# Kernel tuning notes

Measured on AMD Instinct MI355X. Metric: run time of the kernel, lower is better.

Reference implementation:

```python
import jax, jax.numpy as jnp
import numpy as np

MAX_DIST = 3          # census patch radius -> 7x7 neighborhood
PATCH = 2 * MAX_DIST + 1


def _warp(img, flow):
    """Bilinear warp (Resample2d): sample img at (x + u, y + v). Coords clamped to border."""
    B, C, H, W = img.shape
    gy, gx = jnp.meshgrid(jnp.arange(H, dtype=img.dtype), jnp.arange(W, dtype=img.dtype), indexing='ij')
    x = gx[None] + flow[:, 0]           # [B,H,W]
    y = gy[None] + flow[:, 1]
    x0 = jnp.floor(x); y0 = jnp.floor(y)
    wx = x - x0; wy = y - y0            # bilinear weights
    x0i = jnp.clip(x0, 0, W - 1).astype(jnp.int32)
    x1i = jnp.clip(x0 + 1.0, 0, W - 1).astype(jnp.int32)
    y0i = jnp.clip(y0, 0, H - 1).astype(jnp.int32)
    y1i = jnp.clip(y0 + 1.0, 0, H - 1).astype(jnp.int32)

    def gather(im_b, yi, xi):           # im_b [C,H,W], yi/xi [H,W] -> [C,H,W]
        return im_b[:, yi, xi]
    g = jax.vmap(gather)
    Ia = g(img, y0i, x0i); Ib = g(img, y0i, x1i)
    Ic = g(img, y1i, x0i); Id = g(img, y1i, x1i)
    wx = wx[:, None]; wy = wy[:, None]  # [B,1,H,W]
    return Ia * (1 - wx) * (1 - wy) + Ib * wx * (1 - wy) + Ic * (1 - wx) * wy + Id * wx * wy


def _census_transform(image):
    """Ternary census transform: grayscale, extract 7x7 patches, normalized center differences."""
    gray = (0.299 * image[:, 0:1] + 0.587 * image[:, 1:2] + 0.114 * image[:, 2:3]) * 255.0
    w = jnp.eye(PATCH * PATCH, dtype=image.dtype).reshape(PATCH * PATCH, 1, PATCH, PATCH)
    patches = jax.lax.conv_general_dilated(
        gray, w, window_strides=(1, 1), padding=[(MAX_DIST, MAX_DIST)] * 2,
        dimension_numbers=('NCHW', 'OIHW', 'NCHW'))   # [B,49,H,W]
    t = patches - gray
    return t / jnp.sqrt(0.81 + t * t)


def _border_mask(B, H, W, dtype):
    m = jnp.zeros((H, W), dtype).at[MAX_DIST:H - MAX_DIST, MAX_DIST:W - MAX_DIST].set(1.0)
    return jnp.broadcast_to(m[None, None], (B, 1, H, W))


def _charbonnier(x, mask, alpha=0.45, eps=0.001):
    err = (x * x + eps * eps) ** alpha * mask
    return jnp.sum(err) / x.size


def _census_loss(im1, im2_warped, mask):
    t1 = _census_transform(im1)
    t2 = _census_transform(im2_warped)
    d = (t1 - t2) ** 2
    dist = jnp.sum(d / (0.1 + d), axis=1, keepdims=True)   # soft Hamming distance [B,1,H,W]
    B, _, H, W = dist.shape
    return _charbonnier(dist, mask * _border_mask(B, H, W, dist.dtype))


def setup_inputs() -> dict:
    key = jax.random.key(0)
    ks = jax.random.split(key, 6)
    B, H, W = 4, 320, 768
    return {
        'former': jax.random.uniform(ks[0], (B, 3, H, W), jnp.float32),
        'latter': jax.random.uniform(ks[1], (B, 3, H, W), jnp.float32),
        'disp_est_scale': jax.random.normal(ks[2], (B, 2, H, W), jnp.float32) * 3.0,
        'disp_est_scale_2': jax.random.normal(ks[3], (B, 2, H, W), jnp.float32) * 3.0,
        'fw_mask': jax.random.uniform(ks[4], (B, 1, H, W), jnp.float32),
        'bw_mask': jax.random.uniform(ks[5], (B, 1, H, W), jnp.float32),
    }


def reference(former, latter, disp_est_scale, disp_est_scale_2, fw_mask, bw_mask):
    left_est = _warp(latter, disp_est_scale)
    image_loss = _census_loss(former, left_est, fw_mask)
    right_est = _warp(former, disp_est_scale_2)
    image_loss_2 = _census_loss(latter, right_est, bw_mask)
    return (image_loss, image_loss_2)
```

## Files before the change

### kernel.cpp

```cpp
#include <hip/hip_runtime.h>

#define BB 4
#define H 320
#define W 768
#define P (H*W)
#define NPIX (BB*P)

#define TX 32
#define TY 8
#define TW (TX+6)
#define TH (TY+6)
#define HALO (TW*TH)
#define NBX (W/TX)
#define NBY (H/TY)
#define NBLK (NBX*NBY*BB)

__global__ void gray_kernel(const float* __restrict__ former,
                            const float* __restrict__ latter,
                            float* __restrict__ gf, float* __restrict__ gl) {
    int idx = blockIdx.x * blockDim.x + threadIdx.x;
    if (idx >= NPIX) return;
    int b = idx / P;
    int r = idx - b * P;
    const float* f = former + (size_t)b * 3 * P + r;
    const float* l = latter + (size_t)b * 3 * P + r;
    gf[idx] = (0.299f * f[0] + 0.587f * f[P] + 0.114f * f[2 * P]) * 255.f;
    gl[idx] = (0.299f * l[0] + 0.587f * l[P] + 0.114f * l[2 * P]) * 255.f;
}

__device__ __forceinline__ float bilinear(const float* __restrict__ img, float fx, float fy) {
    float x0 = floorf(fx), y0 = floorf(fy);
    float wx = fx - x0, wy = fy - y0;
    float x0c = fminf(fmaxf(x0,       0.f), (float)(W - 1));
    float x1c = fminf(fmaxf(x0 + 1.f, 0.f), (float)(W - 1));
    float y0c = fminf(fmaxf(y0,       0.f), (float)(H - 1));
    float y1c = fminf(fmaxf(y0 + 1.f, 0.f), (float)(H - 1));
    int x0i = (int)x0c, x1i = (int)x1c, y0i = (int)y0c, y1i = (int)y1c;
    float Ia = img[y0i * W + x0i], Ib = img[y0i * W + x1i];
    float Ic = img[y1i * W + x0i], Id = img[y1i * W + x1i];
    float omx = 1.f - wx, omy = 1.f - wy;
    return Ia * omx * omy + Ib * wx * omy + Ic * omx * wy + Id * wx * wy;
}

__global__ __launch_bounds__(256)
void fused_kernel(const float* __restrict__ gf, const float* __restrict__ gl,
                  const float* __restrict__ flow1, const float* __restrict__ flow2,
                  const float* __restrict__ fw_mask, const float* __restrict__ bw_mask,
                  float* __restrict__ partials) {
    __shared__ float sA[HALO], sB[HALO], sC[HALO], sD[HALO];
    const int b   = blockIdx.z;
    const int tx0 = blockIdx.x * TX;
    const int ty0 = blockIdx.y * TY;
    const int tid = threadIdx.x;

    const float* pGF = gf + (size_t)b * P;
    const float* pGL = gl + (size_t)b * P;
    const float* pF1 = flow1 + (size_t)b * 2 * P;
    const float* pF2 = flow2 + (size_t)b * 2 * P;

    for (int i = tid; i < HALO; i += 256) {
        int ly = i / TW, lx = i - ly * TW;
        int gx = min(max(tx0 - 3 + lx, 0), W - 1);
        int gy = min(max(ty0 - 3 + ly, 0), H - 1);
        int o = gy * W + gx;
        sA[i] = pGF[o];
        sC[i] = pGL[o];
        float u1 = pF1[o], v1 = pF1[P + o];
        float u2 = pF2[o], v2 = pF2[P + o];
        sB[i] = bilinear(pGL, (float)gx + u1, (float)gy + v1);
        sD[i] = bilinear(pGF, (float)gx + u2, (float)gy + v2);
    }
    __syncthreads();

    const int lx = tid & 31, ly = tid >> 5;
    const int x = tx0 + lx, y = ty0 + ly;
    float sum1 = 0.f, sum2 = 0.f;

    if (x >= 3 && x < W - 3 && y >= 3 && y < H - 3) {
        const int c = (ly + 3) * TW + (lx + 3);
        const float c1 = sA[c], c2 = sB[c], c3 = sC[c], c4 = sD[c];
        float dist1 = 0.f, dist2 = 0.f;
#pragma unroll
        for (int dy = 0; dy < 7; ++dy) {
            const int ro = (ly + dy) * TW + lx;
            float a[7], bv[7], cv[7], dv[7];
#pragma unroll
            for (int dx = 0; dx < 7; ++dx) { a[dx] = sA[ro + dx]; bv[dx] = sB[ro + dx]; }
#pragma unroll
            for (int dx = 0; dx < 7; ++dx) { cv[dx] = sC[ro + dx]; dv[dx] = sD[ro + dx]; }
#pragma unroll
            for (int dx = 0; dx < 7; ++dx) {
                float t1 = a[dx] - c1;
                float t2 = bv[dx] - c2;
                t1 *= __builtin_amdgcn_rsqf(0.81f + t1 * t1);
                t2 *= __builtin_amdgcn_rsqf(0.81f + t2 * t2);
                float d = t1 - t2; d *= d;
                dist1 += d * __builtin_amdgcn_rcpf(0.1f + d);
            }
#pragma unroll
            for (int dx = 0; dx < 7; ++dx) {
                float t3 = cv[dx] - c3;
                float t4 = dv[dx] - c4;
                t3 *= __builtin_amdgcn_rsqf(0.81f + t3 * t3);
                t4 *= __builtin_amdgcn_rsqf(0.81f + t4 * t4);
                float d = t3 - t4; d *= d;
                dist2 += d * __builtin_amdgcn_rcpf(0.1f + d);
            }
        }
        const float m1 = fw_mask[(size_t)b * P + y * W + x];
        const float m2 = bw_mask[(size_t)b * P + y * W + x];
        sum1 = exp2f(0.45f * log2f(dist1 * dist1 + 1e-6f)) * m1;
        sum2 = exp2f(0.45f * log2f(dist2 * dist2 + 1e-6f)) * m2;
    }

#pragma unroll
    for (int off = 32; off; off >>= 1) {
        sum1 += __shfl_down(sum1, off, 64);
        sum2 += __shfl_down(sum2, off, 64);
    }
    __shared__ float red[8];
    const int wave = tid >> 6, lane = tid & 63;
    if (lane == 0) { red[wave] = sum1; red[4 + wave] = sum2; }
    __syncthreads();
    if (tid == 0) {
        const int blk = (blockIdx.z * NBY + blockIdx.y) * NBX + blockIdx.x;
        partials[2 * blk]     = red[0] + red[1] + red[2] + red[3];
        partials[2 * blk + 1] = red[4] + red[5] + red[6] + red[7];
    }
}

__global__ __launch_bounds__(256)
void reduce_kernel(const float* __restrict__ partials, float* __restrict__ out) {
    const int tid = threadIdx.x;
    float s1 = 0.f, s2 = 0.f;
    for (int i = tid; i < NBLK; i += 256) {
        s1 += partials[2 * i];
        s2 += partials[2 * i + 1];
    }
#pragma unroll
    for (int off = 32; off; off >>= 1) {
        s1 += __shfl_down(s1, off, 64);
        s2 += __shfl_down(s2, off, 64);
    }
    __shared__ float red[8];
    const int wave = tid >> 6, lane = tid & 63;
    if (lane == 0) { red[wave] = s1; red[4 + wave] = s2; }
    __syncthreads();
    if (tid == 0) {
        out[0] = (red[0] + red[1] + red[2] + red[3]) * (1.0f / NPIX);
        out[1] = (red[4] + red[5] + red[6] + red[7]) * (1.0f / NPIX);
    }
}

extern "C" void kernel_launch(void* const* d_in, const int* in_sizes, int n_in,
                              void* d_out, int out_size, void* d_ws, size_t ws_size,
                              hipStream_t stream) {
    (void)in_sizes; (void)n_in; (void)out_size; (void)ws_size;
    const float* former  = (const float*)d_in[0];
    const float* latter  = (const float*)d_in[1];
    const float* flow1   = (const float*)d_in[2];
    const float* flow2   = (const float*)d_in[3];
    const float* fw_mask = (const float*)d_in[4];
    const float* bw_mask = (const float*)d_in[5];
    float* out = (float*)d_out;
    float* ws  = (float*)d_ws;
    float* gf       = ws;
    float* gl       = ws + NPIX;
    float* partials = ws + 2 * (size_t)NPIX;

    gray_kernel<<<(NPIX + 255) / 256, 256, 0, stream>>>(former, latter, gf, gl);
    fused_kernel<<<dim3(NBX, NBY, BB), 256, 0, stream>>>(gf, gl, flow1, flow2,
                                                         fw_mask, bw_mask, partials);
    reduce_kernel<<<1, 256, 0, stream>>>(partials, out);
}
```

Baseline: 139.9 us.

## Merge census math into one rsqrt, pack float2 lanes, vectorize gray, atomic reduce

The per-neighbor ternary census math is rewritten so the two normalizations share one rsqrt of the product q1*q2, with the squared difference expanded algebraically. Both losses are computed in float2 pairs to allow packed FP32 ops, and shared memory is interleaved as float2 arrays. The gray kernel now uses float4 loads and stores, and the separate reduction kernel is replaced by per-block atomicAdds into an output zeroed by the gray kernel. This removes transcendental work and one launch, at the cost of nondeterministic float summation order and slightly different rounding.

```diff
diff --git a/kernel.cpp b/kernel.cpp
--- a/kernel.cpp
+++ b/kernel.cpp
@@ -13,19 +13,48 @@
 #define HALO (TW*TH)
 #define NBX (W/TX)
 #define NBY (H/TY)
-#define NBLK (NBX*NBY*BB)
+
+__device__ __forceinline__ float2 f2(float x, float y) { return make_float2(x, y); }
+__device__ __forceinline__ float2 operator+(float2 a, float2 b) { return f2(a.x + b.x, a.y + b.y); }
+__device__ __forceinline__ float2 operator-(float2 a, float2 b) { return f2(a.x - b.x, a.y - b.y); }
+__device__ __forceinline__ float2 operator*(float2 a, float2 b) { return f2(a.x * b.x, a.y * b.y); }
+__device__ __forceinline__ float2 pk_fma(float2 a, float2 b, float2 c) {
+    return f2(fmaf(a.x, b.x, c.x), fmaf(a.y, b.y, c.y));
+}
+__device__ __forceinline__ float2 pk_fma_s(float s, float2 b, float2 c) {
+    return f2(fmaf(s, b.x, c.x), fmaf(s, b.y, c.y));
+}
+__device__ __forceinline__ float2 pk_add_s(float2 a, float s) { return f2(a.x + s, a.y + s); }
 
 __global__ void gray_kernel(const float* __restrict__ former,
                             const float* __restrict__ latter,
-                            float* __restrict__ gf, float* __restrict__ gl) {
+                            float* __restrict__ gf, float* __restrict__ gl,
+                            float* __restrict__ out) {
     int idx = blockIdx.x * blockDim.x + threadIdx.x;
-    if (idx >= NPIX) return;
-    int b = idx / P;
-    int r = idx - b * P;
+    if (idx == 0) { out[0] = 0.f; out[1] = 0.f; }
+    if (idx >= NPIX / 4) return;
+    int idx4 = idx * 4;
+    int b = idx4 / P;
+    int r = idx4 - b * P;
     const float* f = former + (size_t)b * 3 * P + r;
     const float* l = latter + (size_t)b * 3 * P + r;
-    gf[idx] = (0.299f * f[0] + 0.587f * f[P] + 0.114f * f[2 * P]) * 255.f;
-    gl[idx] = (0.299f * l[0] + 0.587f * l[P] + 0.114f * l[2 * P]) * 255.f;
+    float4 fr = *(const float4*)f;
+    float4 fg = *(const float4*)(f + P);
+    float4 fb = *(const float4*)(f + 2 * P);
+    float4 lr = *(const float4*)l;
+    float4 lg = *(const float4*)(l + P);
+    float4 lb = *(const float4*)(l + 2 * P);
+    float4 og, ol;
+    og.x = (0.299f * fr.x + 0.587f * fg.x + 0.114f * fb.x) * 255.f;
+    og.y = (0.299f * fr.y + 0.587f * fg.y + 0.114f * fb.y) * 255.f;
+    og.z = (0.299f * fr.z + 0.587f * fg.z + 0.114f * fb.z) * 255.f;
+    og.w = (0.299f * fr.w + 0.587f * fg.w + 0.114f * fb.w) * 255.f;
+    ol.x = (0.299f * lr.x + 0.587f * lg.x + 0.114f * lb.x) * 255.f;
+    ol.y = (0.299f * lr.y + 0.587f * lg.y + 0.114f * lb.y) * 255.f;
+    ol.z = (0.299f * lr.z + 0.587f * lg.z + 0.114f * lb.z) * 255.f;
+    ol.w = (0.299f * lr.w + 0.587f * lg.w + 0.114f * lb.w) * 255.f;
+    *(float4*)(gf + idx4) = og;
+    *(float4*)(gl + idx4) = ol;
 }
 
 __device__ __forceinline__ float bilinear(const float* __restrict__ img, float fx, float fy) {
@@ -46,8 +75,9 @@
 void fused_kernel(const float* __restrict__ gf, const float* __restrict__ gl,
                   const float* __restrict__ flow1, const float* __restrict__ flow2,
                   const float* __restrict__ fw_mask, const float* __restrict__ bw_mask,
-                  float* __restrict__ partials) {
-    __shared__ float sA[HALO], sB[HALO], sC[HALO], sD[HALO];
+                  float* __restrict__ out) {
+    __shared__ float2 sAC[HALO];
+    __shared__ float2 sBD[HALO];
     const int b   = blockIdx.z;
     const int tx0 = blockIdx.x * TX;
     const int ty0 = blockIdx.y * TY;
@@ -63,92 +93,70 @@
         int gx = min(max(tx0 - 3 + lx, 0), W - 1);
         int gy = min(max(ty0 - 3 + ly, 0), H - 1);
         int o = gy * W + gx;
-        sA[i] = pGF[o];
-        sC[i] = pGL[o];
+        sAC[i] = f2(pGF[o], pGL[o]);
         float u1 = pF1[o], v1 = pF1[P + o];
         float u2 = pF2[o], v2 = pF2[P + o];
-        sB[i] = bilinear(pGL, (float)gx + u1, (float)gy + v1);
-        sD[i] = bilinear(pGF, (float)gx + u2, (float)gy + v2);
+        sBD[i] = f2(bilinear(pGL, (float)gx + u1, (float)gy + v1),
+                    bilinear(pGF, (float)gx + u2, (float)gy + v2));
     }
     __syncthreads();
 
     const int lx = tid & 31, ly = tid >> 5;
     const int x = tx0 + lx, y = ty0 + ly;
-    float sum1 = 0.f, sum2 = 0.f;
+    float2 sum = f2(0.f, 0.f);
 
     if (x >= 3 && x < W - 3 && y >= 3 && y < H - 3) {
         const int c = (ly + 3) * TW + (lx + 3);
-        const float c1 = sA[c], c2 = sB[c], c3 = sC[c], c4 = sD[c];
-        float dist1 = 0.f, dist2 = 0.f;
+        const float2 cAC = sAC[c], cBD = sBD[c];
+        float2 dist = f2(0.f, 0.f);
 #pragma unroll
         for (int dy = 0; dy < 7; ++dy) {
             const int ro = (ly + dy) * TW + lx;
-            float a[7], bv[7], cv[7], dv[7];
+            float2 ac[7], bd[7];
 #pragma unroll
-            for (int dx = 0; dx < 7; ++dx) { a[dx] = sA[ro + dx]; bv[dx] = sB[ro + dx]; }
+            for (int dx = 0; dx < 7; ++dx) { ac[dx] = sAC[ro + dx]; }
 #pragma unroll
-            for (int dx = 0; dx < 7; ++dx) { cv[dx] = sC[ro + dx]; dv[dx] = sD[ro + dx]; }
+            for (int dx = 0; dx < 7; ++dx) { bd[dx] = sBD[ro + dx]; }
 #pragma unroll
             for (int dx = 0; dx < 7; ++dx) {
-                float t1 = a[dx] - c1;
-                float t2 = bv[dx] - c2;
-                t1 *= __builtin_amdgcn_rsqf(0.81f + t1 * t1);
-                t2 *= __builtin_amdgcn_rsqf(0.81f + t2 * t2);
-                float d = t1 - t2; d *= d;
-                dist1 += d * __builtin_amdgcn_rcpf(0.1f + d);
-            }
-#pragma unroll
-            for (int dx = 0; dx < 7; ++dx) {
-                float t3 = cv[dx] - c3;
-                float t4 = dv[dx] - c4;
-                t3 *= __builtin_amdgcn_rsqf(0.81f + t3 * t3);
-                t4 *= __builtin_amdgcn_rsqf(0.81f + t4 * t4);
-                float d = t3 - t4; d *= d;
-                dist2 += d * __builtin_amdgcn_rcpf(0.1f + d);
+                float2 a = ac[dx] - cAC;
+                float2 bb = bd[dx] - cBD;
+                float2 q1 = pk_fma(a, a, f2(0.81f, 0.81f));
+                float2 q2 = pk_fma(bb, bb, f2(0.81f, 0.81f));
+                float2 Q  = q1 * q2;
+                float2 R  = f2(__builtin_amdgcn_rsqf(Q.x), __builtin_amdgcn_rsqf(Q.y));
+                float2 Pp = R * R;
+                float2 ab = a * bb;
+                float2 S  = q1 + q2;
+                float2 h  = S * Pp;
+                float2 g  = pk_fma_s(-0.81f, h, f2(2.f, 2.f));
+                float2 v  = ab * R;
+                float2 d  = pk_fma_s(-2.f, v, g);
+                float2 e  = pk_add_s(d, 0.1f);
+                float2 r  = f2(__builtin_amdgcn_rcpf(e.x), __builtin_amdgcn_rcpf(e.y));
+                dist = pk_fma(d, r, dist);
             }
         }
         const float m1 = fw_mask[(size_t)b * P + y * W + x];
         const float m2 = bw_mask[(size_t)b * P + y * W + x];
-        sum1 = exp2f(0.45f * log2f(dist1 * dist1 + 1e-6f)) * m1;
-        sum2 = exp2f(0.45f * log2f(dist2 * dist2 + 1e-6f)) * m2;
+        sum.x = exp2f(0.45f * log2f(fmaf(dist.x, dist.x, 1e-6f))) * m1;
+        sum.y = exp2f(0.45f * log2f(fmaf(dist.y, dist.y, 1e-6f))) * m2;
     }
 
 #pragma unroll
     for (int off = 32; off; off >>= 1) {
-        sum1 += __shfl_down(sum1, off, 64);
-        sum2 += __shfl_down(sum2, off, 64);
+        sum.x += __shfl_down(sum.x, off, 64);
+        sum.y += __shfl_down(sum.y, off, 64);
     }
     __shared__ float red[8];
     const int wave = tid >> 6, lane = tid & 63;
-    if (lane == 0) { red[wave] = sum1; red[4 + wave] = sum2; }
+    if (lane == 0) { red[wave] = sum.x; red[4 + wave] = sum.y; }
     __syncthreads();
     if (tid == 0) {
-        const int blk = (blockIdx.z * NBY + blockIdx.y) * NBX + blockIdx.x;
-        partials[2 * blk]     = red[0] + red[1] + red[2] + red[3];
-        partials[2 * blk + 1] = red[4] + red[5] + red[6] + red[7];
-    }
-}
-
-__global__ __launch_bounds__(256)
-void reduce_kernel(const float* __restrict__ partials, float* __restrict__ out) {
-    const int tid = threadIdx.x;
-    float s1 = 0.f, s2 = 0.f;
-    for (int i = tid; i < NBLK; i += 256) {
-        s1 += partials[2 * i];
-        s2 += partials[2 * i + 1];
-    }
-#pragma unroll
-    for (int off = 32; off; off >>= 1) {
-        s1 += __shfl_down(s1, off, 64);
-        s2 += __shfl_down(s2, off, 64);
-    }
-    __shared__ float red[8];
-    const int wave = tid >> 6, lane = tid & 63;
-    if (lane == 0) { red[wave] = s1; red[4 + wave] = s2; }
-    __syncthreads();
-    if (tid == 0) {
-        out[0] = (red[0] + red[1] + red[2] + red[3]) * (1.0f / NPIX);
-        out[1] = (red[4] + red[5] + red[6] + red[7]) * (1.0f / NPIX);
+        float s1 = red[0] + red[1] + red[2] + red[3];
+        float s2 = red[4] + red[5] + red[6] + red[7];
+        atomicAdd(&out[0], s1 * (1.0f / NPIX));
+        atomicAdd(&out[1], s2 * (1.0f / NPIX));
     }
 }
 
@@ -164,12 +172,10 @@
     const float* bw_mask = (const float*)d_in[5];
     float* out = (float*)d_out;
     float* ws  = (float*)d_ws;
-    float* gf       = ws;
-    float* gl       = ws + NPIX;
-    float* partials = ws + 2 * (size_t)NPIX;
+    float* gf  = ws;
+    float* gl  = ws + NPIX;
 
-    gray_kernel<<<(NPIX + 255) / 256, 256, 0, stream>>>(former, latter, gf, gl);
+    gray_kernel<<<(NPIX / 4 + 255) / 256, 256, 0, stream>>>(former, latter, gf, gl, out);
     fused_kernel<<<dim3(NBX, NBY, BB), 256, 0, stream>>>(gf, gl, flow1, flow2,
-                                                         fw_mask, bw_mask, partials);
-    reduce_kernel<<<1, 256, 0, stream>>>(partials, out);
+                                                         fw_mask, bw_mask, out);
 }
```

Result: slower. 196.4 us (+40.4%).
